# Kernel optimization log

Hardware: AMD Instinct MI355X
Metric: run time of the kernel (lower is better)

Reference implementation:

```python
import jax, jax.numpy as jnp
import numpy as np

D_MODEL = 1024
NHEAD = 16
HEAD_DIM = D_MODEL // NHEAD
EPS = 1e-5


def _layer_norm(x, gamma, beta):
    mu = jnp.mean(x, axis=-1, keepdims=True)
    var = jnp.mean(jnp.square(x - mu), axis=-1, keepdims=True)
    return (x - mu) * jax.lax.rsqrt(var + EPS) * gamma + beta


def setup_inputs() -> dict:
    key = jax.random.key(0)
    ks = jax.random.split(key, 8)
    s = 1.0 / np.sqrt(D_MODEL)
    return {
        "x": jax.random.normal(ks[0], (4, 2048, D_MODEL), dtype=jnp.float32),
        "Wq": jax.random.uniform(ks[1], (D_MODEL, D_MODEL), jnp.float32, -s, s),
        "Wk": jax.random.uniform(ks[2], (D_MODEL, D_MODEL), jnp.float32, -s, s),
        "Wv": jax.random.uniform(ks[3], (D_MODEL, D_MODEL), jnp.float32, -s, s),
        "ln1_g": jnp.ones((D_MODEL,), jnp.float32),
        "ln1_b": jnp.zeros((D_MODEL,), jnp.float32),
        "ln2_g": jnp.ones((D_MODEL,), jnp.float32),
        "ln2_b": jnp.zeros((D_MODEL,), jnp.float32),
        "W1": jax.random.uniform(ks[4], (D_MODEL, D_MODEL), jnp.float32, -s, s),
        "b1": jax.random.uniform(ks[5], (D_MODEL,), jnp.float32, -s, s),
        "W2": jax.random.uniform(ks[6], (D_MODEL, D_MODEL), jnp.float32, -s, s),
        "b2": jax.random.uniform(ks[7], (D_MODEL,), jnp.float32, -s, s),
    }


def reference(x, Wq, Wk, Wv, ln1_g, ln1_b, ln2_g, ln2_b, W1, b1, W2, b2):
    B, S, D = x.shape
    temperature = jnp.sqrt(jnp.asarray(D_MODEL / NHEAD, x.dtype))
    xn = _layer_norm(x, ln1_g, ln1_b)
    # torch Linear: y = x @ W.T (weights are [out, in], no bias for q/k/v)
    q = (xn @ Wq.T).reshape(B, S, NHEAD, HEAD_DIM)
    k = (xn @ Wk.T).reshape(B, S, NHEAD, HEAD_DIM)
    v = (xn @ Wv.T).reshape(B, S, NHEAD, HEAD_DIM)
    scores = jnp.einsum("bqhd,bkhd->bhqk", q, k) / temperature  # [B,H,S,S]
    causal = jnp.tril(jnp.ones((S, S), dtype=bool))
    scores = jnp.where(causal, scores, jnp.asarray(-jnp.inf, scores.dtype))
    attn = jax.nn.softmax(scores, axis=-1)
    att_out = jnp.einsum("bhqk,bkhd->bqhd", attn, v).reshape(B, S, D)
    xt = x + att_out
    xt2 = _layer_norm(xt, ln2_g, ln2_b)
    ffn = jax.nn.relu(xt2 @ W1.T + b1) @ W2.T + b2  # dropout=0 -> identity
    return xt + ffn
```

## Files before the change

### kernel.cpp

```cpp
#include <hip/hip_runtime.h>
#include <hip/hip_bf16.h>

typedef unsigned short u16;
typedef unsigned int u32;
typedef __attribute__((ext_vector_type(8))) __bf16 bf16x8;
typedef __attribute__((ext_vector_type(4))) float f32x4;
typedef __attribute__((ext_vector_type(16))) float f32x16;
typedef __attribute__((ext_vector_type(8))) unsigned short ushort8v;
typedef __attribute__((ext_vector_type(4))) unsigned short u16x4;
typedef __attribute__((ext_vector_type(4))) unsigned int u32x4;

#define DEV __device__ __forceinline__
#define AS1 __attribute__((address_space(1)))
#define AS3 __attribute__((address_space(3)))

DEV u16 f2bf(float f) {
    union { float f; unsigned int i; } u; u.f = f;
    unsigned int x = u.i;
    unsigned int r = (x + 0x7fffu + ((x >> 16) & 1u)) >> 16;
    return (u16)r;
}
DEV float bf2f(u16 h) {
    union { unsigned int i; float f; } u; u.i = ((unsigned int)h) << 16;
    return u.f;
}
DEV u32 cvt_pk_bf16(float lo, float hi) {
    u32 r;
    asm("v_cvt_pk_bf16_f32 %0, %1, %2" : "=v"(r) : "v"(lo), "v"(hi));
    return r;
}
DEV void pl32swap(u32& a, u32& b) {
    asm volatile("v_permlane32_swap_b32 %0, %1" : "+v"(a), "+v"(b));
}

__global__ __launch_bounds__(256) void ln1_cvt(
    const float* __restrict__ xin,
    const float* __restrict__ g, const float* __restrict__ be,
    u16* __restrict__ y_bf,
    const float* __restrict__ wq, const float* __restrict__ wk,
    const float* __restrict__ wv, const float* __restrict__ w1,
    const float* __restrict__ w2, u16* __restrict__ wdst)
{
    const int tid = threadIdx.x;
    if (blockIdx.x >= 8192) {
        const int i = ((blockIdx.x - 8192) * 256 + tid) * 4;
        auto conv4 = [](float4 a, float s) {
            u16x4 r; r[0] = f2bf(a.x * s); r[1] = f2bf(a.y * s);
            r[2] = f2bf(a.z * s); r[3] = f2bf(a.w * s);
            return r;
        };
        const float qs = 0.125f * 1.44269504f;
        *(u16x4*)(wdst + i)               = conv4(*(const float4*)(wq + i), qs);
        *(u16x4*)(wdst + (1 << 20) + i)   = conv4(*(const float4*)(wk + i), 1.0f);
        *(u16x4*)(wdst + (2 << 20) + i)   = conv4(*(const float4*)(wv + i), 1.0f);
        *(u16x4*)(wdst + (3 << 20) + i)   = conv4(*(const float4*)(w1 + i), 1.0f);
        *(u16x4*)(wdst + (4 << 20) + i)   = conv4(*(const float4*)(w2 + i), 1.0f);
        return;
    }
    const int row = blockIdx.x;
    const size_t base = (size_t)row * 1024 + tid * 4;
    float4 xv = *(const float4*)(xin + base);
    float v[4] = {xv.x, xv.y, xv.z, xv.w};
    float s = 0.f, ss = 0.f;
    #pragma unroll
    for (int j = 0; j < 4; ++j) { s += v[j]; ss += v[j] * v[j]; }
    #pragma unroll
    for (int o = 32; o > 0; o >>= 1) { s += __shfl_xor(s, o); ss += __shfl_xor(ss, o); }
    __shared__ float red[8];
    const int w = tid >> 6;
    if ((tid & 63) == 0) { red[w * 2] = s; red[w * 2 + 1] = ss; }
    __syncthreads();
    s  = red[0] + red[2] + red[4] + red[6];
    ss = red[1] + red[3] + red[5] + red[7];
    const float mu = s * (1.0f / 1024.0f);
    const float var = ss * (1.0f / 1024.0f) - mu * mu;
    const float rstd = rsqrtf(var + 1e-5f);
    const int col = tid * 4;
    float4 gv = *(const float4*)(g + col);
    float4 bv = *(const float4*)(be + col);
    u16x4 o4;
    o4[0] = f2bf((v[0] - mu) * rstd * gv.x + bv.x);
    o4[1] = f2bf((v[1] - mu) * rstd * gv.y + bv.y);
    o4[2] = f2bf((v[2] - mu) * rstd * gv.z + bv.z);
    o4[3] = f2bf((v[3] - mu) * rstd * gv.w + bv.w);
    *(u16x4*)(y_bf + base) = o4;
}

__global__ __launch_bounds__(256) void ln2_kernel(
    const float* __restrict__ xin, const u16* __restrict__ addbf,
    const float* __restrict__ g, const float* __restrict__ be,
    u16* __restrict__ xt_out, u16* __restrict__ y_bf)
{
    const int row = blockIdx.x;
    const int tid = threadIdx.x;
    const size_t base = (size_t)row * 1024 + tid * 4;

    float4 xv = *(const float4*)(xin + base);
    float v[4] = {xv.x, xv.y, xv.z, xv.w};
    u16x4 a = *(const u16x4*)(addbf + base);
    v[0] += bf2f(a[0]); v[1] += bf2f(a[1]); v[2] += bf2f(a[2]); v[3] += bf2f(a[3]);
    u16x4 o;
    o[0] = f2bf(v[0]); o[1] = f2bf(v[1]); o[2] = f2bf(v[2]); o[3] = f2bf(v[3]);
    *(u16x4*)(xt_out + base) = o;

    float s = 0.f, ss = 0.f;
    #pragma unroll
    for (int j = 0; j < 4; ++j) { s += v[j]; ss += v[j] * v[j]; }
    #pragma unroll
    for (int o2 = 32; o2 > 0; o2 >>= 1) { s += __shfl_xor(s, o2); ss += __shfl_xor(ss, o2); }
    __shared__ float red[8];
    const int w = tid >> 6;
    if ((tid & 63) == 0) { red[w * 2] = s; red[w * 2 + 1] = ss; }
    __syncthreads();
    s  = red[0] + red[2] + red[4] + red[6];
    ss = red[1] + red[3] + red[5] + red[7];
    const float mu = s * (1.0f / 1024.0f);
    const float var = ss * (1.0f / 1024.0f) - mu * mu;
    const float rstd = rsqrtf(var + 1e-5f);

    const int col = tid * 4;
    float4 gv = *(const float4*)(g + col);
    float4 bv = *(const float4*)(be + col);
    u16x4 o4;
    o4[0] = f2bf((v[0] - mu) * rstd * gv.x + bv.x);
    o4[1] = f2bf((v[1] - mu) * rstd * gv.y + bv.y);
    o4[2] = f2bf((v[2] - mu) * rstd * gv.z + bv.z);
    o4[3] = f2bf((v[3] - mu) * rstd * gv.w + bv.w);
    *(u16x4*)(y_bf + base) = o4;
}

template<int EPI>
__global__ __launch_bounds__(256, 4) void gemm_bt(
    const u16* __restrict__ A, const u16* __restrict__ Bt,
    void* __restrict__ Cout, const float* __restrict__ bias,
    const u16* __restrict__ resid, int M, int N, int K)
{
    __shared__ u16 As[2 * 128 * 32];
    __shared__ u16 Bs[2 * 128 * 32];
    const int tid = threadIdx.x;
    const int l = tid & 63;
    const int w = tid >> 6;
    const int wm = w >> 1, wn = w & 1;
    const int fr = l & 15, fc = l >> 4;
    const size_t rowA0 = (size_t)blockIdx.x * 128;
    const size_t rowB0 = (size_t)blockIdx.y * 128;

    f32x4 acc[4][4] = {};
    const int ldoff = fr * 32 + fc * 8;

    const int nkt = K >> 6;
    for (int kt = 0; kt < nkt; ++kt) {
        __syncthreads();
        const int k0 = kt << 6;
        #pragma unroll
        for (int q = 0; q < 4; ++q) {
            const int row = (q & 1) * 64 + w * 16 + (l >> 2);
            const int kk  = (q >> 1) * 32 + (l & 3) * 8;
            const u16* ga = A  + (rowA0 + row) * K + k0 + kk;
            const u16* gb = Bt + (rowB0 + row) * K + k0 + kk;
            u16* da = As + q * 2048 + w * 512;
            u16* db = Bs + q * 2048 + w * 512;
            __builtin_amdgcn_global_load_lds((const AS1 void*)ga, (AS3 void*)da, 16, 0, 0);
            __builtin_amdgcn_global_load_lds((const AS1 void*)gb, (AS3 void*)db, 16, 0, 0);
        }
        __syncthreads();
        #pragma unroll
        for (int ks = 0; ks < 2; ++ks) {
            const u16* as_p = As + ks * 4096;
            const u16* bs_p = Bs + ks * 4096;
            bf16x8 af[4], bfv[4];
            #pragma unroll
            for (int m = 0; m < 4; ++m)
                af[m] = *(const bf16x8*)(as_p + (wm * 64 + m * 16) * 32 + ldoff);
            #pragma unroll
            for (int n = 0; n < 4; ++n)
                bfv[n] = *(const bf16x8*)(bs_p + (wn * 64 + n * 16) * 32 + ldoff);
            #pragma unroll
            for (int m = 0; m < 4; ++m)
                #pragma unroll
                for (int n = 0; n < 4; ++n)
                    acc[m][n] = __builtin_amdgcn_mfma_f32_16x16x32_bf16(
                        af[m], bfv[n], acc[m][n], 0, 0, 0);
        }
    }

    const int r0 = (int)rowA0 + wm * 64;
    const int c0 = (int)rowB0 + wn * 64;
    #pragma unroll
    for (int m = 0; m < 4; ++m) {
        #pragma unroll
        for (int n = 0; n < 4; ++n) {
            const int rowbase = r0 + m * 16 + fc * 4;
            const int col = c0 + n * 16 + fr;
            if constexpr (EPI == 0) {
                const int which = col >> 10;
                const int hh = (col >> 6) & 15;
                const int dd = col & 63;
                const size_t hb2 = (size_t)(rowbase >> 11) * 16 + hh;
                const int s0 = rowbase & 2047;
                if (which == 2) {
                    u16x4 pk;
                    #pragma unroll
                    for (int j = 0; j < 4; ++j) pk[j] = f2bf(acc[m][n][j]);
                    *(u16x4*)((u16*)Cout + (size_t)2 * 8388608 +
                              (hb2 * 64 + dd) * 2048 + s0) = pk;
                } else {
                    #pragma unroll
                    for (int j = 0; j < 4; ++j)
                        ((u16*)Cout)[(size_t)which * 8388608 +
                                     (hb2 * 2048 + s0 + j) * 64 + dd] =
                            f2bf(acc[m][n][j]);
                }
            } else {
                #pragma unroll
                for (int j = 0; j < 4; ++j) {
                    float v = acc[m][n][j];
                    const size_t idx = (size_t)(rowbase + j) * N + col;
                    if constexpr (EPI == 1) {
                        v += bias[col];
                        v = fmaxf(v, 0.0f);
                        ((u16*)Cout)[idx] = f2bf(v);
                    } else {
                        v += bias[col] + bf2f(resid[idx]);
                        ((float*)Cout)[idx] = v;
                    }
                }
            }
        }
    }
}

__global__ __launch_bounds__(256, 4) void attn_fwd(
    const u16* __restrict__ Qh, const u16* __restrict__ Kh,
    const u16* __restrict__ Vh, u16* __restrict__ attout)
{
    __shared__ u16 Ks[2][64 * 64];
    __shared__ u16 Vt[2][64 * 64];

    const int bid = blockIdx.x;
    const int pair = (bid >> 3) & 15;
    const int g = (bid & 7) + 8 * (bid >> 7);
    const int h = g & 15, b = g >> 4;

    const int tid = threadIdx.x, l = tid & 63, w = tid >> 6;
    const int lq = l & 31, hi = l >> 5, hi8 = hi * 8;
    const int qhalf = w & 1, kvblk = w >> 1;
    const int kvb32 = kvblk * 32;
    const int hb = b * 16 + h;
    const size_t head = (size_t)hb << 17;
    const u16* kb_g = Kh + head;
    const u16* vb_g = Vh + head;

    const int swr = (lq & 7) << 3;

    const int grow0 = w * 16 + (l >> 3);
    const int gsw   = ((l & 7) * 8) ^ ((l >> 3) << 3);

    #pragma unroll 1
    for (int half = 0; half < 2; ++half) {
        const int qt = half ? 31 - pair : pair;
        const int qbw = qt * 64 + qhalf * 32;
        const int qg = qbw + lq;

        bf16x8 qf[4];
        {
            const u16* qp = Qh + head + (size_t)(qbw + lq) * 64 + hi8;
            #pragma unroll
            for (int ds = 0; ds < 4; ++ds)
                qf[ds] = *(const bf16x8*)(qp + ds * 16);
        }

        f32x16 acc[2] = {};
        float l_part = 0.0f;

        const int nkt = qt + 1;
        int cur = 0;

        #pragma unroll
        for (int i = 0; i < 2; ++i) {
            const int row = grow0 + i * 8;
            __builtin_amdgcn_global_load_lds(
                (const AS1 void*)(kb_g + (size_t)row * 64 + gsw),
                (AS3 void*)(&Ks[0][0] + (w * 16 + i * 8) * 64), 16, 0, 0);
            __builtin_amdgcn_global_load_lds(
                (const AS1 void*)(vb_g + (size_t)row * 2048 + gsw),
                (AS3 void*)(&Vt[0][0] + (w * 16 + i * 8) * 64), 16, 0, 0);
        }
        __builtin_amdgcn_sched_barrier(0);
        asm volatile("s_waitcnt vmcnt(0)" ::: "memory");
        __builtin_amdgcn_s_barrier();

        #pragma unroll 1
        for (int kt = 0; kt < nkt; ++kt) {
            const int kv0 = kt * 64;
            const bool diag = (kt == qt);
            const u16* ksc = &Ks[cur][0];
            const u16* vtc = &Vt[cur][0];

            if (kt + 1 < nkt) {
                u16* ksn = &Ks[cur ^ 1][0];
                u16* vtn = &Vt[cur ^ 1][0];
                #pragma unroll
                for (int i = 0; i < 2; ++i) {
                    const int row = grow0 + i * 8;
                    __builtin_amdgcn_global_load_lds(
                        (const AS1 void*)(kb_g + (size_t)(kv0 + 64 + row) * 64 + gsw),
                        (AS3 void*)(ksn + (w * 16 + i * 8) * 64), 16, 0, 0);
                    __builtin_amdgcn_global_load_lds(
                        (const AS1 void*)(vb_g + (size_t)row * 2048 + kv0 + 64 + gsw),
                        (AS3 void*)(vtn + (w * 16 + i * 8) * 64), 16, 0, 0);
                }
            }
            __builtin_amdgcn_sched_barrier(0);

            if (!(diag && qhalf == 0 && kvblk == 1)) {
                f32x16 sa = {};
                const u16* kbase = ksc + (kvb32 + lq) * 64;
                __builtin_amdgcn_s_setprio(1);
                #pragma unroll
                for (int ds = 0; ds < 4; ++ds) {
                    const bf16x8 kf = *(const bf16x8*)(kbase + ((ds * 16 + hi8) ^ swr));
                    sa = __builtin_amdgcn_mfma_f32_32x32x16_bf16(kf, qf[ds], sa, 0, 0, 0);
                }
                __builtin_amdgcn_s_setprio(0);

                if (diag && kvblk == qhalf) {
                    const int kvbase = kv0 + kvb32 + 4 * hi;
                    #pragma unroll
                    for (int r = 0; r < 16; ++r) {
                        const int kg = kvbase + (r & 3) + 8 * (r >> 2);
                        if (kg > qg) sa[r] = -3.0e38f;
                    }
                }

                float ls = 0.0f;
                #pragma unroll
                for (int r = 0; r < 16; ++r) { sa[r] = exp2f(sa[r]); ls += sa[r]; }
                l_part += ls;

                u32 P0 = cvt_pk_bf16(sa[0],  sa[1]);
                u32 P1 = cvt_pk_bf16(sa[2],  sa[3]);
                u32 P2 = cvt_pk_bf16(sa[4],  sa[5]);
                u32 P3 = cvt_pk_bf16(sa[6],  sa[7]);
                u32 P4 = cvt_pk_bf16(sa[8],  sa[9]);
                u32 P5 = cvt_pk_bf16(sa[10], sa[11]);
                u32 P6 = cvt_pk_bf16(sa[12], sa[13]);
                u32 P7 = cvt_pk_bf16(sa[14], sa[15]);
                pl32swap(P0, P2); pl32swap(P1, P3);
                pl32swap(P4, P6); pl32swap(P5, P7);
                u32x4 w0v = {P0, P1, P2, P3};
                u32x4 w1v = {P4, P5, P6, P7};
                const bf16x8 pf0 = __builtin_bit_cast(bf16x8, w0v);
                const bf16x8 pf1 = __builtin_bit_cast(bf16x8, w1v);

                __builtin_amdgcn_s_setprio(1);
                #pragma unroll
                for (int dblk = 0; dblk < 2; ++dblk) {
                    const u16* vbase = vtc + (lq + dblk * 32) * 64;
                    const bf16x8 vf0 = *(const bf16x8*)(vbase + ((kvb32 + hi8) ^ swr));
                    acc[dblk] = __builtin_amdgcn_mfma_f32_32x32x16_bf16(
                        vf0, pf0, acc[dblk], 0, 0, 0);
                    const bf16x8 vf1 = *(const bf16x8*)(vbase + ((kvb32 + 16 + hi8) ^ swr));
                    acc[dblk] = __builtin_amdgcn_mfma_f32_32x32x16_bf16(
                        vf1, pf1, acc[dblk], 0, 0, 0);
                }
                __builtin_amdgcn_s_setprio(0);
            }

            __builtin_amdgcn_sched_barrier(0);
            asm volatile("s_waitcnt vmcnt(0)" ::: "memory");
            asm volatile("s_waitcnt lgkmcnt(0)" ::: "memory");
            __builtin_amdgcn_s_barrier();
            cur ^= 1;
        }

        float* accs = (float*)&Ks[0][0];
        float* lsh  = (float*)&Vt[0][0];
        if (kvblk == 1) {
            float* rgn = accs + qhalf * 2048;
            #pragma unroll
            for (int e = 0; e < 16; ++e) {
                rgn[e * 64 + l]        = acc[0][e];
                rgn[(16 + e) * 64 + l] = acc[1][e];
            }
            lsh[qhalf * 64 + l] = l_part;
        }
        __syncthreads();
        if (kvblk == 0) {
            const float* rgn = accs + qhalf * 2048;
            #pragma unroll
            for (int e = 0; e < 16; ++e) {
                acc[0][e] += rgn[e * 64 + l];
                acc[1][e] += rgn[(16 + e) * 64 + l];
            }
            l_part += lsh[qhalf * 64 + l];
            const float l_tot = l_part + __shfl_xor(l_part, 32);
            const float inv = 1.0f / l_tot;
            const size_t obase = ((size_t)b * 2048 + qbw + lq) * 1024 + h * 64;
            #pragma unroll
            for (int dblk = 0; dblk < 2; ++dblk) {
                #pragma unroll
                for (int gq = 0; gq < 4; ++gq) {
                    u16x4 o;
                    #pragma unroll
                    for (int j = 0; j < 4; ++j)
                        o[j] = f2bf(acc[dblk][4 * gq + j] * inv);
                    *(u16x4*)(attout + obase + dblk * 32 + gq * 8 + 4 * hi) = o;
                }
            }
        }
        __syncthreads();
    }
}

extern "C" void kernel_launch(void* const* d_in, const int* in_sizes, int n_in,
                              void* d_out, int out_size, void* d_ws, size_t ws_size,
                              hipStream_t stream)
{
    const float* x    = (const float*)d_in[0];
    const float* Wq   = (const float*)d_in[1];
    const float* Wk   = (const float*)d_in[2];
    const float* Wv   = (const float*)d_in[3];
    const float* ln1g = (const float*)d_in[4];
    const float* ln1b = (const float*)d_in[5];
    const float* ln2g = (const float*)d_in[6];
    const float* ln2b = (const float*)d_in[7];
    const float* W1   = (const float*)d_in[8];
    const float* b1   = (const float*)d_in[9];
    const float* W2   = (const float*)d_in[10];
    const float* b2   = (const float*)d_in[11];

    char* ws = (char*)d_ws;
    u16*   wbf  = (u16*)(ws);
    u16*   xn   = (u16*)(ws + 10485760);
    u16*   qkvb = (u16*)(ws + 27262976);
    u16*   attb = (u16*)(ws + 77594624);
    u16*   xt   = (u16*)(ws + 94371840);

    ln1_cvt<<<9216, 256, 0, stream>>>(x, ln1g, ln1b, xn, Wq, Wk, Wv, W1, W2, wbf);
    gemm_bt<0><<<dim3(64, 24), 256, 0, stream>>>(xn, wbf, qkvb, nullptr, nullptr,
                                                 8192, 3072, 1024);
    attn_fwd<<<1024, 256, 0, stream>>>(qkvb, qkvb + 8388608, qkvb + 16777216, attb);
    ln2_kernel<<<8192, 256, 0, stream>>>(x, attb, ln2g, ln2b, xt, xn);
    gemm_bt<1><<<dim3(64, 8), 256, 0, stream>>>(xn, wbf + (3 << 20), qkvb, b1, nullptr,
                                                8192, 1024, 1024);
    gemm_bt<2><<<dim3(64, 8), 256, 0, stream>>>(qkvb, wbf + (4 << 20), d_out, b2, xt,
                                                8192, 1024, 1024);
}
```

Baseline: 208.0 us.

## Triple-buffer K tiles and stagger K/V prefetch in attention loop

```diff
diff --git a/kernel.cpp b/kernel.cpp
--- a/kernel.cpp
+++ b/kernel.cpp
@@ -234,7 +234,7 @@
     const u16* __restrict__ Qh, const u16* __restrict__ Kh,
     const u16* __restrict__ Vh, u16* __restrict__ attout)
 {
-    __shared__ u16 Ks[2][64 * 64];
+    __shared__ u16 Ks[3][64 * 64];
     __shared__ u16 Vt[2][64 * 64];
 
     const int bid = blockIdx.x;
@@ -256,6 +256,25 @@
     const int grow0 = w * 16 + (l >> 3);
     const int gsw   = ((l & 7) * 8) ^ ((l >> 3) << 3);
 
+    auto stageK = [&](int kt, int buf) {
+        #pragma unroll
+        for (int i = 0; i < 2; ++i) {
+            const int row = grow0 + i * 8;
+            __builtin_amdgcn_global_load_lds(
+                (const AS1 void*)(kb_g + (size_t)(kt * 64 + row) * 64 + gsw),
+                (AS3 void*)(&Ks[buf][0] + (w * 16 + i * 8) * 64), 16, 0, 0);
+        }
+    };
+    auto stageV = [&](int kt, int buf) {
+        #pragma unroll
+        for (int i = 0; i < 2; ++i) {
+            const int row = grow0 + i * 8;
+            __builtin_amdgcn_global_load_lds(
+                (const AS1 void*)(vb_g + (size_t)row * 2048 + kt * 64 + gsw),
+                (AS3 void*)(&Vt[buf][0] + (w * 16 + i * 8) * 64), 16, 0, 0);
+        }
+    };
+
     #pragma unroll 1
     for (int half = 0; half < 2; ++half) {
         const int qt = half ? 31 - pair : pair;
@@ -274,44 +293,24 @@
         float l_part = 0.0f;
 
         const int nkt = qt + 1;
-        int cur = 0;
-
-        #pragma unroll
-        for (int i = 0; i < 2; ++i) {
-            const int row = grow0 + i * 8;
-            __builtin_amdgcn_global_load_lds(
-                (const AS1 void*)(kb_g + (size_t)row * 64 + gsw),
-                (AS3 void*)(&Ks[0][0] + (w * 16 + i * 8) * 64), 16, 0, 0);
-            __builtin_amdgcn_global_load_lds(
-                (const AS1 void*)(vb_g + (size_t)row * 2048 + gsw),
-                (AS3 void*)(&Vt[0][0] + (w * 16 + i * 8) * 64), 16, 0, 0);
-        }
-        __builtin_amdgcn_sched_barrier(0);
-        asm volatile("s_waitcnt vmcnt(0)" ::: "memory");
-        __builtin_amdgcn_s_barrier();
-
+
+        stageK(0, 0);
+        stageV(0, 0);
+        if (nkt > 1) stageK(1, 1);
+
+        int kb = 0;
         #pragma unroll 1
         for (int kt = 0; kt < nkt; ++kt) {
+            if (kt + 1 < nkt) asm volatile("s_waitcnt vmcnt(2)" ::: "memory");
+            else              asm volatile("s_waitcnt vmcnt(0)" ::: "memory");
+            __builtin_amdgcn_s_barrier();
+            if (kt + 1 < nkt) stageV(kt + 1, (kt + 1) & 1);
+            __builtin_amdgcn_sched_barrier(0);
+
             const int kv0 = kt * 64;
             const bool diag = (kt == qt);
-            const u16* ksc = &Ks[cur][0];
-            const u16* vtc = &Vt[cur][0];
-
-            if (kt + 1 < nkt) {
-                u16* ksn = &Ks[cur ^ 1][0];
-                u16* vtn = &Vt[cur ^ 1][0];
-                #pragma unroll
-                for (int i = 0; i < 2; ++i) {
-                    const int row = grow0 + i * 8;
-                    __builtin_amdgcn_global_load_lds(
-                        (const AS1 void*)(kb_g + (size_t)(kv0 + 64 + row) * 64 + gsw),
-                        (AS3 void*)(ksn + (w * 16 + i * 8) * 64), 16, 0, 0);
-                    __builtin_amdgcn_global_load_lds(
-                        (const AS1 void*)(vb_g + (size_t)row * 2048 + kv0 + 64 + gsw),
-                        (AS3 void*)(vtn + (w * 16 + i * 8) * 64), 16, 0, 0);
-                }
-            }
-            __builtin_amdgcn_sched_barrier(0);
+            const u16* ksc = &Ks[kb][0];
+            const u16* vtc = &Vt[kt & 1][0];
 
             if (!(diag && qhalf == 0 && kvblk == 1)) {
                 f32x16 sa = {};
@@ -367,12 +366,14 @@
                 __builtin_amdgcn_s_setprio(0);
             }
 
+            if (kt + 2 < nkt) {
+                int kb2 = kb + 2; if (kb2 >= 3) kb2 -= 3;
+                stageK(kt + 2, kb2);
+            }
             __builtin_amdgcn_sched_barrier(0);
-            asm volatile("s_waitcnt vmcnt(0)" ::: "memory");
-            asm volatile("s_waitcnt lgkmcnt(0)" ::: "memory");
-            __builtin_amdgcn_s_barrier();
-            cur ^= 1;
-        }
+            ++kb; if (kb == 3) kb = 0;
+        }
+        __syncthreads();
 
         float* accs = (float*)&Ks[0][0];
         float* lsh  = (float*)&Vt[0][0];
```

Result: no change. 209.1 us (+0.5%).
